# Optimization experiments

Hardware: AMD Instinct MI355X
Metric: run time of the kernel (lower is better)

## Reference

```python
import jax, jax.numpy as jnp
import numpy as np

B, S, DM, H = 4, 4096, 1024, 16
DEPTH = DM // H  # 64


def setup_inputs() -> dict:
    key = jax.random.key(0)
    ks = jax.random.split(key, 11)
    scale = 1.0 / np.sqrt(DM)
    inp = {
        "Q": jax.random.normal(ks[0], (B, S, DM), dtype=jnp.float32),
        "K": jax.random.normal(ks[1], (B, S, DM), dtype=jnp.float32),
        "V": jax.random.normal(ks[2], (B, S, DM), dtype=jnp.float32),
        "mask": jnp.zeros((B, S, H, H), dtype=jnp.float32),
        "Wq": jax.random.normal(ks[3], (DM, DM), dtype=jnp.float32) * scale,
        "bq": jnp.zeros((DM,), dtype=jnp.float32),
        "Wk": jax.random.normal(ks[4], (DM, DM), dtype=jnp.float32) * scale,
        "bk": jnp.zeros((DM,), dtype=jnp.float32),
        "Wv": jax.random.normal(ks[5], (DM, DM), dtype=jnp.float32) * scale,
        "bv": jnp.zeros((DM,), dtype=jnp.float32),
        "Wo": jax.random.normal(ks[6], (DM, DM), dtype=jnp.float32) * scale,
        "bo": jnp.zeros((DM,), dtype=jnp.float32),
    }
    return inp


def reference(Q, K, V, mask, Wq, bq, Wk, bk, Wv, bv, Wo, bo):
    # QKV projections
    q = (Q @ Wq + bq).reshape(B, S, H, DEPTH)
    k = (K @ Wk + bk).reshape(B, S, H, DEPTH)
    v = (V @ Wv + bv).reshape(B, S, H, DEPTH)
    # NOTE: source never applies the [0,2,1,3] transpose, so attention is
    # computed across the HEAD axis per token: scores are [B,S,H,H].
    scores = jnp.einsum('bshd,bsgd->bshg', q, k) / jnp.sqrt(jnp.float32(DEPTH))
    scores = scores + mask * (-1e9)
    weights = jax.nn.softmax(scores, axis=-1)
    attn = jnp.einsum('bshg,bsgd->bshd', weights, v)  # [B,S,H,DEPTH]
    concat = attn.reshape(B, S, DM)
    output = concat @ Wo + bo
    return (output, output)
```

## Files before the change

### kernel.cpp

```cpp
#include <hip/hip_runtime.h>


typedef __attribute__((ext_vector_type(8))) short bf16x8;
typedef __attribute__((ext_vector_type(4))) float f32x4;

#define MTOK 16384
#define KDIM 1024
#define OUT_HALF 16777216

static __device__ __forceinline__ unsigned short f2bf(float f) {
  unsigned u = __float_as_uint(f);
  u += 0x7FFFu + ((u >> 16) & 1u);
  return (unsigned short)(u >> 16);
}

static __device__ __forceinline__ void gload_lds16(const void* g, void* l) {
  __builtin_amdgcn_global_load_lds(
      (const __attribute__((address_space(1))) unsigned*)g,
      (__attribute__((address_space(3))) unsigned*)l, 16, 0, 0);
}

__global__ __launch_bounds__(256) void castk(const float* __restrict__ in,
                                             unsigned short* __restrict__ out,
                                             int n8) {
  int i = blockIdx.x * 256 + threadIdx.x;
  if (i >= n8) return;
  const float4* p = (const float4*)in + (size_t)i * 2;
  float4 x = p[0], y = p[1];
  bf16x8 o;
  o[0] = f2bf(x.x); o[1] = f2bf(x.y); o[2] = f2bf(x.z); o[3] = f2bf(x.w);
  o[4] = f2bf(y.x); o[5] = f2bf(y.y); o[6] = f2bf(y.z); o[7] = f2bf(y.w);
  *(bf16x8*)(out + (size_t)i * 8) = o;
}

__global__ __launch_bounds__(256) void wtrans(const float* __restrict__ W0,
                                              const float* __restrict__ W1,
                                              const float* __restrict__ W2,
                                              const float* __restrict__ W3,
                                              unsigned short* __restrict__ Wt) {
  __shared__ float tile[64][65];
  int w = blockIdx.y;
  const float* W = (w == 0) ? W0 : (w == 1) ? W1 : (w == 2) ? W2 : W3;
  unsigned short* dst = Wt + (size_t)w * (1024 * 1024);
  int tkb = (blockIdx.x >> 4) * 64;
  int tnb = (blockIdx.x & 15) * 64;
  int tx = threadIdx.x & 63, ty = threadIdx.x >> 6;
#pragma unroll
  for (int p = 0; p < 16; ++p) {
    int k = ty + p * 4;
    tile[k][tx] = W[(size_t)(tkb + k) * 1024 + tnb + tx];
  }
  __syncthreads();
#pragma unroll
  for (int p = 0; p < 16; ++p) {
    int n = ty + p * 4;
    dst[(size_t)(tnb + n) * 1024 + tkb + tx] = f2bf(tile[tx][n]);
  }
}

template <int MODE>
__global__ __launch_bounds__(256) void gemm_bt(
    const unsigned short* __restrict__ A, const unsigned short* __restrict__ Bt,
    const float* __restrict__ bias, unsigned short* __restrict__ Cbf,
    float* __restrict__ Cf) {
  __shared__ unsigned short ldsA[2][128 * 32];
  __shared__ unsigned short ldsB[2][128 * 32];
  const int tid = threadIdx.x;
  const int lane = tid & 63;
  const int wid = tid >> 6;
  const int l15 = lane & 15, gp = lane >> 4;
  const int wr = (wid >> 1) * 64, wc = (wid & 1) * 64;
  const long brow = (long)blockIdx.y * 128;
  const long bcol = (long)blockIdx.x * 128;

  const int j0 = tid, j1 = 256 + tid;
  const int r0 = j0 >> 2, b0 = (j0 & 3) ^ (r0 & 3);
  const int r1 = j1 >> 2, b1 = (j1 & 3) ^ (r1 & 3);
  const unsigned short* gA0 = A + (brow + r0) * KDIM + b0 * 8;
  const unsigned short* gA1 = A + (brow + r1) * KDIM + b1 * 8;
  const unsigned short* gB0 = Bt + (bcol + r0) * KDIM + b0 * 8;
  const unsigned short* gB1 = Bt + (bcol + r1) * KDIM + b1 * 8;
  const unsigned ldsOff0 = (unsigned)(wid * 64) * 8;
  const unsigned ldsOff1 = (unsigned)(256 + wid * 64) * 8;

  f32x4 acc[4][4];
#pragma unroll
  for (int m = 0; m < 4; ++m)
#pragma unroll
    for (int n = 0; n < 4; ++n) acc[m][n] = (f32x4){0.f, 0.f, 0.f, 0.f};

  auto stage = [&](int buf, int kt) {
    const int ko = kt * 32;
    gload_lds16(gA0 + ko, &ldsA[buf][ldsOff0]);
    gload_lds16(gA1 + ko, &ldsA[buf][ldsOff1]);
    gload_lds16(gB0 + ko, &ldsB[buf][ldsOff0]);
    gload_lds16(gB1 + ko, &ldsB[buf][ldsOff1]);
  };

  unsigned aoff[4], boff[4];
#pragma unroll
  for (int m = 0; m < 4; ++m) {
    int row = wr + m * 16 + l15;
    aoff[m] = (unsigned)(row * 32 + ((gp ^ (row & 3)) * 8));
    int col = wc + m * 16 + l15;
    boff[m] = (unsigned)(col * 32 + ((gp ^ (col & 3)) * 8));
  }

  stage(0, 0);
  for (int kt = 0; kt < 32; ++kt) {
    __syncthreads();
    if (kt + 1 < 32) stage((kt + 1) & 1, kt + 1);
    const int cur = kt & 1;
    bf16x8 a[4], b[4];
#pragma unroll
    for (int m = 0; m < 4; ++m) a[m] = *(const bf16x8*)&ldsA[cur][aoff[m]];
#pragma unroll
    for (int n = 0; n < 4; ++n) b[n] = *(const bf16x8*)&ldsB[cur][boff[n]];
#pragma unroll
    for (int m = 0; m < 4; ++m)
#pragma unroll
      for (int n = 0; n < 4; ++n)
        acc[m][n] = __builtin_amdgcn_mfma_f32_16x16x32_bf16(a[m], b[n],
                                                            acc[m][n], 0, 0, 0);
  }

#pragma unroll
  for (int n = 0; n < 4; ++n) {
    const long col = bcol + wc + n * 16 + l15;
    const float bv = bias[col];
#pragma unroll
    for (int m = 0; m < 4; ++m) {
#pragma unroll
      for (int r = 0; r < 4; ++r) {
        const long row = brow + wr + m * 16 + gp * 4 + r;
        const float v = acc[m][n][r] + bv;
        if constexpr (MODE == 0) {
          Cbf[row * KDIM + col] = f2bf(v);
        } else {
          Cf[row * KDIM + col] = v;
          Cf[row * KDIM + col + OUT_HALF] = v;
        }
      }
    }
  }
}

__global__ __launch_bounds__(256) void attn_k(
    const unsigned short* __restrict__ qb, const unsigned short* __restrict__ kb,
    const unsigned short* __restrict__ vb, const float* __restrict__ mask,
    unsigned short* __restrict__ attn) {
  const int tid = threadIdx.x, lane = tid & 63, w = tid >> 6;
  const long t = (long)blockIdx.x * 4 + w;
  const unsigned short* qr = qb + t * KDIM;
  const unsigned short* kr = kb + t * KDIM;
  const unsigned short* vr = vb + t * KDIM;
  const int l15 = lane & 15, gp = lane >> 4;

  bf16x8 kf0 = *(const bf16x8*)(kr + l15 * 64 + gp * 8);
  bf16x8 kf1 = *(const bf16x8*)(kr + l15 * 64 + 32 + gp * 8);
  bf16x8 qf0 = *(const bf16x8*)(qr + l15 * 64 + gp * 8);
  bf16x8 qf1 = *(const bf16x8*)(qr + l15 * 64 + 32 + gp * 8);
  f32x4 st = {0.f, 0.f, 0.f, 0.f};
  st = __builtin_amdgcn_mfma_f32_16x16x32_bf16(kf0, qf0, st, 0, 0, 0);
  st = __builtin_amdgcn_mfma_f32_16x16x32_bf16(kf1, qf1, st, 0, 0, 0);

  float s[4];
  const float* mrow = mask + t * 256 + l15 * 16 + gp * 4;
#pragma unroll
  for (int r = 0; r < 4; ++r) s[r] = st[r] * 0.125f - 1e9f * mrow[r];

  float mx = fmaxf(fmaxf(s[0], s[1]), fmaxf(s[2], s[3]));
  mx = fmaxf(mx, __shfl_xor(mx, 16, 64));
  mx = fmaxf(mx, __shfl_xor(mx, 32, 64));
  float p[4], sum = 0.f;
#pragma unroll
  for (int r = 0; r < 4; ++r) { p[r] = __expf(s[r] - mx); sum += p[r]; }
  sum += __shfl_xor(sum, 16, 64);
  sum += __shfl_xor(sum, 32, 64);
  const float inv = 1.0f / sum;
#pragma unroll
  for (int r = 0; r < 4; ++r) p[r] *= inv;

  bf16x8 pa;
#pragma unroll
  for (int i = 0; i < 8; ++i) {
    const int g = gp * 8 + i;
    const int src = l15 + 16 * ((g >> 2) & 3);
    const float v = __shfl(p[i & 3], src, 64);
    pa[i] = (gp < 2) ? (short)f2bf(v) : (short)0;
  }

#pragma unroll
  for (int nb = 0; nb < 4; ++nb) {
    bf16x8 vf;
#pragma unroll
    for (int i = 0; i < 8; ++i) {
      const int g = gp * 8 + i;
      vf[i] = (gp < 2) ? (short)vr[g * 64 + nb * 16 + l15] : (short)0;
    }
    f32x4 o = {0.f, 0.f, 0.f, 0.f};
    o = __builtin_amdgcn_mfma_f32_16x16x32_bf16(pa, vf, o, 0, 0, 0);
#pragma unroll
    for (int r = 0; r < 4; ++r) {
      const int h = gp * 4 + r;
      attn[t * KDIM + h * 64 + nb * 16 + l15] = f2bf(o[r]);
    }
  }
}

extern "C" void kernel_launch(void* const* d_in, const int* in_sizes, int n_in,
                              void* d_out, int out_size, void* d_ws,
                              size_t ws_size, hipStream_t stream) {
  const float* Q  = (const float*)d_in[0];
  const float* K  = (const float*)d_in[1];
  const float* V  = (const float*)d_in[2];
  const float* mask = (const float*)d_in[3];
  const float* Wq = (const float*)d_in[4];
  const float* bq = (const float*)d_in[5];
  const float* Wk = (const float*)d_in[6];
  const float* bk = (const float*)d_in[7];
  const float* Wv = (const float*)d_in[8];
  const float* bv = (const float*)d_in[9];
  const float* Wo = (const float*)d_in[10];
  const float* bo = (const float*)d_in[11];
  float* out = (float*)d_out;

  const size_t EL = (size_t)MTOK * KDIM;
  unsigned short* Cb = (unsigned short*)d_ws;
  unsigned short* qb = Cb + EL;
  unsigned short* kb = qb + EL;
  unsigned short* vb = kb + EL;
  unsigned short* Wt = vb + EL;

  const size_t need = (4 * EL + 4ul * 1024 * 1024) * 2;
  if (ws_size < need) return;

  dim3 b256(256);
  dim3 gg(8, 128);

  wtrans<<<dim3(256, 4), b256, 0, stream>>>(Wq, Wk, Wv, Wo, Wt);

  castk<<<8192, b256, 0, stream>>>(Q, Cb, 2097152);
  gemm_bt<0><<<gg, b256, 0, stream>>>(Cb, Wt + 0 * 1048576, bq, qb, nullptr);
  castk<<<8192, b256, 0, stream>>>(K, Cb, 2097152);
  gemm_bt<0><<<gg, b256, 0, stream>>>(Cb, Wt + 1 * 1048576, bk, kb, nullptr);
  castk<<<8192, b256, 0, stream>>>(V, Cb, 2097152);
  gemm_bt<0><<<gg, b256, 0, stream>>>(Cb, Wt + 2 * 1048576, bv, vb, nullptr);

  attn_k<<<4096, b256, 0, stream>>>(qb, kb, vb, mask, Cb);

  gemm_bt<1><<<gg, b256, 0, stream>>>(Cb, Wt + 3 * 1048576, bo, nullptr, out);
}
```

Before: 590.6 us.

## Batch QKV casts and GEMMs into single launches, stage attention V/output through LDS

Merges the three cast kernels into one 3D-grid launch and the three QKV projection GEMMs into one grouped launch over 3072 workgroups. The grouped launch remaps workgroup IDs so consecutive blocks are spread across XCDs, which is meant to cut launch count and tail effects and improve L2 locality. In the attention kernel, V is loaded with 16-byte vector loads into swizzled LDS and the output is staged through LDS so it can be written with wide coalesced stores instead of scattered 2-byte accesses. The workspace grows to hold separate cast buffers for Q, K and V.

```diff
diff --git a/kernel.cpp b/kernel.cpp
--- a/kernel.cpp
+++ b/kernel.cpp
@@ -20,11 +20,14 @@
       (__attribute__((address_space(3))) unsigned*)l, 16, 0, 0);
 }
 
-__global__ __launch_bounds__(256) void castk(const float* __restrict__ in,
-                                             unsigned short* __restrict__ out,
-                                             int n8) {
+__global__ __launch_bounds__(256) void castk3(
+    const float* __restrict__ Q, const float* __restrict__ K,
+    const float* __restrict__ V, unsigned short* __restrict__ Qb,
+    unsigned short* __restrict__ Kb, unsigned short* __restrict__ Vb) {
+  const int z = blockIdx.y;
+  const float* in = (z == 0) ? Q : (z == 1) ? K : V;
+  unsigned short* out = (z == 0) ? Qb : (z == 1) ? Kb : Vb;
   int i = blockIdx.x * 256 + threadIdx.x;
-  if (i >= n8) return;
   const float4* p = (const float4*)in + (size_t)i * 2;
   float4 x = p[0], y = p[1];
   bf16x8 o;
@@ -58,20 +61,33 @@
   }
 }
 
-template <int MODE>
+template <int MODE, int NWG>
 __global__ __launch_bounds__(256) void gemm_bt(
-    const unsigned short* __restrict__ A, const unsigned short* __restrict__ Bt,
-    const float* __restrict__ bias, unsigned short* __restrict__ Cbf,
+    const unsigned short* __restrict__ A0, const unsigned short* __restrict__ A1,
+    const unsigned short* __restrict__ A2, const unsigned short* __restrict__ Btb,
+    const float* __restrict__ bias0, const float* __restrict__ bias1,
+    const float* __restrict__ bias2, unsigned short* __restrict__ O0,
+    unsigned short* __restrict__ O1, unsigned short* __restrict__ O2,
     float* __restrict__ Cf) {
   __shared__ unsigned short ldsA[2][128 * 32];
   __shared__ unsigned short ldsB[2][128 * 32];
+
+  const int wid = blockIdx.x + (blockIdx.y << 3) + (blockIdx.z << 10);
+  const int rid = (wid & 7) * (NWG >> 3) + (wid >> 3);
+  const int bx = rid & 7, by = (rid >> 3) & 127, z = rid >> 10;
+
+  const unsigned short* A = (z == 0) ? A0 : (z == 1) ? A1 : A2;
+  const unsigned short* Bt = Btb + (size_t)z * 1048576;
+  const float* bias = (z == 0) ? bias0 : (z == 1) ? bias1 : bias2;
+  unsigned short* Cbf = (z == 0) ? O0 : (z == 1) ? O1 : O2;
+
   const int tid = threadIdx.x;
   const int lane = tid & 63;
-  const int wid = tid >> 6;
+  const int wid4 = tid >> 6;
   const int l15 = lane & 15, gp = lane >> 4;
-  const int wr = (wid >> 1) * 64, wc = (wid & 1) * 64;
-  const long brow = (long)blockIdx.y * 128;
-  const long bcol = (long)blockIdx.x * 128;
+  const int wr = (wid4 >> 1) * 64, wc = (wid4 & 1) * 64;
+  const long brow = (long)by * 128;
+  const long bcol = (long)bx * 128;
 
   const int j0 = tid, j1 = 256 + tid;
   const int r0 = j0 >> 2, b0 = (j0 & 3) ^ (r0 & 3);
@@ -80,8 +96,8 @@
   const unsigned short* gA1 = A + (brow + r1) * KDIM + b1 * 8;
   const unsigned short* gB0 = Bt + (bcol + r0) * KDIM + b0 * 8;
   const unsigned short* gB1 = Bt + (bcol + r1) * KDIM + b1 * 8;
-  const unsigned ldsOff0 = (unsigned)(wid * 64) * 8;
-  const unsigned ldsOff1 = (unsigned)(256 + wid * 64) * 8;
+  const unsigned ldsOff0 = (unsigned)(wid4 * 64) * 8;
+  const unsigned ldsOff1 = (unsigned)(256 + wid4 * 64) * 8;
 
   f32x4 acc[4][4];
 #pragma unroll
@@ -149,12 +165,23 @@
     const unsigned short* __restrict__ qb, const unsigned short* __restrict__ kb,
     const unsigned short* __restrict__ vb, const float* __restrict__ mask,
     unsigned short* __restrict__ attn) {
+  __shared__ char vlds[4][2048];
   const int tid = threadIdx.x, lane = tid & 63, w = tid >> 6;
+  char* lbuf = vlds[w];
   const long t = (long)blockIdx.x * 4 + w;
   const unsigned short* qr = qb + t * KDIM;
   const unsigned short* kr = kb + t * KDIM;
   const unsigned short* vr = vb + t * KDIM;
   const int l15 = lane & 15, gp = lane >> 4;
+
+  {
+    const int g = lane >> 2, c = lane & 3;
+    uint4 v0 = *(const uint4*)(vr + g * 64 + c * 16);
+    uint4 v1 = *(const uint4*)(vr + g * 64 + c * 16 + 8);
+    const unsigned s = (unsigned)(((g >> 1) & 7) << 4);
+    *(uint4*)(lbuf + (((unsigned)(g * 128 + c * 32)) ^ s)) = v0;
+    *(uint4*)(lbuf + (((unsigned)(g * 128 + c * 32 + 16)) ^ s)) = v1;
+  }
 
   bf16x8 kf0 = *(const bf16x8*)(kr + l15 * 64 + gp * 8);
   bf16x8 kf1 = *(const bf16x8*)(kr + l15 * 64 + 32 + gp * 8);
@@ -190,21 +217,42 @@
     pa[i] = (gp < 2) ? (short)f2bf(v) : (short)0;
   }
 
+  float ov[4][4];
 #pragma unroll
   for (int nb = 0; nb < 4; ++nb) {
     bf16x8 vf;
 #pragma unroll
     for (int i = 0; i < 8; ++i) {
-      const int g = gp * 8 + i;
-      vf[i] = (gp < 2) ? (short)vr[g * 64 + nb * 16 + l15] : (short)0;
+      const int gi = (gp * 8 + i) & 15;
+      const unsigned byte =
+          ((unsigned)(gi * 128 + (nb * 16 + l15) * 2)) ^
+          (unsigned)(((gi >> 1) & 7) << 4);
+      const unsigned short val = *(const unsigned short*)(lbuf + byte);
+      vf[i] = (gp < 2) ? (short)val : (short)0;
     }
     f32x4 o = {0.f, 0.f, 0.f, 0.f};
     o = __builtin_amdgcn_mfma_f32_16x16x32_bf16(pa, vf, o, 0, 0, 0);
 #pragma unroll
+    for (int r = 0; r < 4; ++r) ov[nb][r] = o[r];
+  }
+
+#pragma unroll
+  for (int nb = 0; nb < 4; ++nb)
+#pragma unroll
     for (int r = 0; r < 4; ++r) {
       const int h = gp * 4 + r;
-      attn[t * KDIM + h * 64 + nb * 16 + l15] = f2bf(o[r]);
+      const unsigned byte =
+          ((unsigned)(h * 128 + (nb * 16 + l15) * 2)) ^
+          (unsigned)(((h >> 1) & 7) << 4);
+      *(unsigned short*)(lbuf + byte) = f2bf(ov[nb][r]);
     }
+  {
+    const int h = lane >> 2, c = lane & 3;
+    const unsigned s2 = (unsigned)(((h >> 1) & 7) << 4);
+    uint4 a0 = *(const uint4*)(lbuf + (((unsigned)(h * 128 + c * 32)) ^ s2));
+    uint4 a1 = *(const uint4*)(lbuf + (((unsigned)(h * 128 + c * 32 + 16)) ^ s2));
+    *(uint4*)(attn + t * KDIM + h * 64 + c * 16) = a0;
+    *(uint4*)(attn + t * KDIM + h * 64 + c * 16 + 8) = a1;
   }
 }
 
@@ -226,28 +274,28 @@
   float* out = (float*)d_out;
 
   const size_t EL = (size_t)MTOK * KDIM;
-  unsigned short* Cb = (unsigned short*)d_ws;
-  unsigned short* qb = Cb + EL;
+  unsigned short* Qb = (unsigned short*)d_ws;
+  unsigned short* Kb = Qb + EL;
+  unsigned short* Vb = Kb + EL;
+  unsigned short* qb = Vb + EL;
   unsigned short* kb = qb + EL;
   unsigned short* vb = kb + EL;
   unsigned short* Wt = vb + EL;
-
-  const size_t need = (4 * EL + 4ul * 1024 * 1024) * 2;
+  unsigned short* attnb = Qb;
+
+  const size_t need = (6 * EL + 4ul * 1024 * 1024) * 2;
   if (ws_size < need) return;
 
   dim3 b256(256);
-  dim3 gg(8, 128);
-
   wtrans<<<dim3(256, 4), b256, 0, stream>>>(Wq, Wk, Wv, Wo, Wt);
-
-  castk<<<8192, b256, 0, stream>>>(Q, Cb, 2097152);
-  gemm_bt<0><<<gg, b256, 0, stream>>>(Cb, Wt + 0 * 1048576, bq, qb, nullptr);
-  castk<<<8192, b256, 0, stream>>>(K, Cb, 2097152);
-  gemm_bt<0><<<gg, b256, 0, stream>>>(Cb, Wt + 1 * 1048576, bk, kb, nullptr);
-  castk<<<8192, b256, 0, stream>>>(V, Cb, 2097152);
-  gemm_bt<0><<<gg, b256, 0, stream>>>(Cb, Wt + 2 * 1048576, bv, vb, nullptr);
-
-  attn_k<<<4096, b256, 0, stream>>>(qb, kb, vb, mask, Cb);
-
-  gemm_bt<1><<<gg, b256, 0, stream>>>(Cb, Wt + 3 * 1048576, bo, nullptr, out);
-}
+  castk3<<<dim3(8192, 3), b256, 0, stream>>>(Q, K, V, Qb, Kb, Vb);
+
+  gemm_bt<0, 3072><<<dim3(8, 128, 3), b256, 0, stream>>>(
+      Qb, Kb, Vb, Wt, bq, bk, bv, qb, kb, vb, nullptr);
+
+  attn_k<<<4096, b256, 0, stream>>>(qb, kb, vb, mask, attnb);
+
+  gemm_bt<1, 1024><<<dim3(8, 128, 1), b256, 0, stream>>>(
+      attnb, attnb, attnb, Wt + 3 * 1048576, bo, bo, bo, nullptr, nullptr,
+      nullptr, out);
+}
```

Result: faster. 559.8 us (-5.2%).
